# Kernel optimization log

Measured on AMD Instinct MI355X. Metric: run time of the kernel, lower is better.

The kernel has to match this reference:

```python
import jax, jax.numpy as jnp
import numpy as np

B, N, D, H, K = 8, 1024, 1024, 64, 20


def setup_inputs() -> dict:
    key = jax.random.key(0)
    ks = jax.random.split(key, 8)
    s = 0.05
    return {
        "f1": jax.random.normal(ks[0], (B, N, D), jnp.float32),
        "f2": jax.random.normal(ks[1], (B, N, D), jnp.float32),
        "W1a": jax.random.normal(ks[2], (D, H), jnp.float32) * s,
        "b1a": jnp.zeros((H,), jnp.float32),
        "W2a": jax.random.normal(ks[3], (H, H), jnp.float32) * s,
        "b2a": jnp.zeros((H,), jnp.float32),
        "W1b": jax.random.normal(ks[4], (H, H), jnp.float32) * s,
        "b1b": jnp.zeros((H,), jnp.float32),
        "W2b": jax.random.normal(ks[5], (H, H), jnp.float32) * s,
        "b2b": jnp.zeros((H,), jnp.float32),
        "k": K,
    }


def _knn_idx(f, k):
    # f: [N, D] -> indices [N, k] of k nearest neighbors (self excluded)
    sq = jnp.sum(f * f, axis=-1)                      # [N]
    d = sq[:, None] + sq[None, :] - 2.0 * (f @ f.T)   # [N, N] squared dists
    n = f.shape[0]
    d = d + jnp.eye(n, dtype=f.dtype) * jnp.float32(1e10)  # exclude self-loop
    _, idx = jax.lax.top_k(-d, k)                     # smallest distances
    return idx


def _gin_layer(x, idx, W1, b1, W2, b2):
    # GINConv with eps=0: MLP(x + sum_{j in N(i)} x_j)
    agg = jnp.sum(x[idx], axis=1)                     # [N, D] neighbor-sum
    h = x + agg
    h = jnp.maximum(h @ W1 + b1, 0.0) @ W2 + b2
    return h


def reference(f1, f2, W1a, b1a, W2a, b2a, W1b, b1b, W2b, b2b, k):
    def encode(f):
        idx = _knn_idx(f, k)
        h = _gin_layer(f, idx, W1a, b1a, W2a, b2a)
        h = _gin_layer(h, idx, W1b, b1b, W2b, b2b)
        return h

    def per_sample(a, b):
        z1 = encode(a)                                # [N, H]
        z2 = encode(b)                                # [N, H]
        sim = z1 @ z2.T                               # [N, N]
        return jax.nn.softmax(sim, axis=1)

    return jax.vmap(per_sample)(f1, f2)               # [B, N, N]
```

## Files before the change

### kernel.cpp

```cpp
#include <hip/hip_runtime.h>
#include <hip/hip_bf16.h>
#include <math.h>

#define BATCH 8
#define NPTS  1024
#define DIM   1024
#define HID   64
#define KNN   20
#define NMAT  16
#define KPACK 3072

typedef __attribute__((ext_vector_type(8))) short short8;
typedef __attribute__((ext_vector_type(4))) float floatx4;

__device__ __forceinline__ const float* mat_base(const float* f1, const float* f2, int m) {
    return (m < BATCH) ? (f1 + (size_t)m * NPTS * DIM)
                       : (f2 + (size_t)(m - BATCH) * NPTS * DIM);
}

__device__ __forceinline__ unsigned short f2bf_bits(float v) {
    __hip_bfloat16 h = __float2bfloat16(v);
    return *(unsigned short*)&h;
}
__device__ __forceinline__ float bfbits2f(unsigned short b) {
    union { unsigned u; float f; } c; c.u = ((unsigned)b) << 16; return c.f;
}

__global__ __launch_bounds__(256) void split_kernel(const float* __restrict__ f1,
                                                    const float* __restrict__ f2,
                                                    unsigned short* __restrict__ H,
                                                    float* __restrict__ sq) {
    int tid = threadIdx.x;
    int wave = tid >> 6, lane = tid & 63;
    int row = blockIdx.x * 4 + wave;
    int m = row >> 10, i = row & (NPTS - 1);
    const float* fr = mat_base(f1, f2, m) + (size_t)i * DIM;
    unsigned short* Hr = H + (size_t)row * KPACK;
    float s = 0.f;
    #pragma unroll
    for (int t = 0; t < 4; ++t) {
        int idx = t * 256 + lane * 4;
        float4 v = *(const float4*)&fr[idx];
        s += v.x * v.x + v.y * v.y + v.z * v.z + v.w * v.w;
        unsigned short h1[4], h2[4], h3[4];
        float vv[4] = {v.x, v.y, v.z, v.w};
        #pragma unroll
        for (int c = 0; c < 4; ++c) {
            unsigned short b1 = f2bf_bits(vv[c]);
            float r1 = vv[c] - bfbits2f(b1);
            unsigned short b2 = f2bf_bits(r1);
            float r2 = r1 - bfbits2f(b2);
            unsigned short b3 = f2bf_bits(r2);
            h1[c] = b1; h2[c] = b2; h3[c] = b3;
        }
        *(ushort4*)&Hr[idx]        = *(ushort4*)&h1[0];
        *(ushort4*)&Hr[1024 + idx] = *(ushort4*)&h2[0];
        *(ushort4*)&Hr[2048 + idx] = *(ushort4*)&h3[0];
    }
    #pragma unroll
    for (int o = 32; o > 0; o >>= 1) s += __shfl_down(s, o);
    if (lane == 0) sq[row] = s;
}

__global__ __launch_bounds__(256) void gram_mfma_kernel(const unsigned short* __restrict__ H,
                                                        const float* __restrict__ sq,
                                                        float* __restrict__ dist) {
    int bid = blockIdx.x;
    int xcd = bid & 7;
    int g = bid >> 3;
    int m = xcd + 8 * (g & 1);
    int t = g >> 1;
    int bi = 0;
    { int a = t; while (a >= 8 - bi) { a -= 8 - bi; ++bi; } t = a; }
    int bj = bi + t;
    int ti = bi << 7, tj = bj << 7;

    const unsigned short* Hm = H + (size_t)m * NPTS * KPACK;

    __shared__ __align__(16) unsigned short Asl[24 * 512];
    __shared__ __align__(16) unsigned short Bsl[24 * 512];

    int tid = threadIdx.x;
    int w = tid >> 6, lane = tid & 63;
    int wi = w >> 1, wj = w & 1;
    int r16 = lane & 15, kc = lane >> 4;

    floatx4 acc[4][4];
    #pragma unroll
    for (int a = 0; a < 4; ++a)
        #pragma unroll
        for (int b = 0; b < 4; ++b) acc[a][b] = (floatx4)0.f;

    for (int kk = 0; kk < 1024; kk += 32) {
        __syncthreads();
        #pragma unroll
        for (int c = 0; c < 6; ++c) {
            int ca = w * 6 + c;
            int seg = ca >> 3;
            int rb  = ca & 7;
            size_t koff = (size_t)(seg << 10) + kk + kc * 8;
            const unsigned short* ga = Hm + (size_t)(ti + rb * 16 + r16) * KPACK + koff;
            const unsigned short* gb = Hm + (size_t)(tj + rb * 16 + r16) * KPACK + koff;
            __builtin_amdgcn_global_load_lds(
                (const __attribute__((address_space(1))) void*)ga,
                (__attribute__((address_space(3))) void*)&Asl[ca * 512], 16, 0, 0);
            __builtin_amdgcn_global_load_lds(
                (const __attribute__((address_space(1))) void*)gb,
                (__attribute__((address_space(3))) void*)&Bsl[ca * 512], 16, 0, 0);
        }
        __syncthreads();
        short8 af[3][4];
        #pragma unroll
        for (int s = 0; s < 3; ++s)
            #pragma unroll
            for (int a = 0; a < 4; ++a)
                af[s][a] = *(const short8*)&Asl[(s * 8 + wi * 4 + a) * 512 + lane * 8];
        #pragma unroll
        for (int sb = 0; sb < 3; ++sb) {
            short8 bf[4];
            #pragma unroll
            for (int b = 0; b < 4; ++b)
                bf[b] = *(const short8*)&Bsl[(sb * 8 + wj * 4 + b) * 512 + lane * 8];
            #pragma unroll
            for (int sa = 0; sa < 3; ++sa) {
                if (sa + sb > 2) continue;
                #pragma unroll
                for (int a = 0; a < 4; ++a)
                    #pragma unroll
                    for (int b = 0; b < 4; ++b)
                        acc[a][b] = __builtin_amdgcn_mfma_f32_16x16x32_bf16(af[sa][a], bf[b], acc[a][b], 0, 0, 0);
            }
        }
    }

    const float* sqm = sq + m * NPTS;
    #pragma unroll
    for (int a = 0; a < 4; ++a) {
        int i0 = ti + wi * 64 + a * 16 + (lane >> 4) * 4;
        #pragma unroll
        for (int b = 0; b < 4; ++b) {
            int j = tj + wj * 64 + b * 16 + (lane & 15);
            float sqj = sqm[j];
            #pragma unroll
            for (int r = 0; r < 4; ++r) {
                int i = i0 + r;
                float v = sqm[i] + sqj - 2.f * acc[a][b][r];
                if (i == j) v += 1e10f;
                dist[((size_t)m * NPTS + i) * NPTS + j] = v;
                if (bi != bj) dist[((size_t)m * NPTS + j) * NPTS + i] = v;
            }
        }
    }
}

__global__ __launch_bounds__(256) void topk_kernel(const float* __restrict__ dist,
                                                   int* __restrict__ knn_idx) {
    int tid = threadIdx.x;
    int wave = tid >> 6, lane = tid & 63;
    int row = blockIdx.x * 4 + wave;
    const float* d = dist + (size_t)row * NPTS;
    float v[16];
    #pragma unroll
    for (int s = 0; s < 16; ++s) v[s] = d[s * 64 + lane];
    int myj = 0;
    for (int sel = 0; sel < KNN; ++sel) {
        float bv = v[0]; int bs = 0;
        #pragma unroll
        for (int s = 1; s < 16; ++s)
            if (v[s] < bv) { bv = v[s]; bs = s; }
        int bj = bs * 64 + lane;
        #pragma unroll
        for (int off = 1; off < 64; off <<= 1) {
            float ov = __shfl_xor(bv, off);
            int   oj = __shfl_xor(bj, off);
            if (ov < bv || (ov == bv && oj < bj)) { bv = ov; bj = oj; }
        }
        if ((bj & 63) == lane) v[bj >> 6] = 3e38f;
        if (lane == sel) myj = bj;
    }
    if (lane < KNN) knn_idx[(size_t)row * KNN + lane] = myj;
}

__global__ __launch_bounds__(256) void hsum_big_kernel(const float* __restrict__ f1,
                                                       const float* __restrict__ f2,
                                                       const int* __restrict__ knn_idx,
                                                       float* __restrict__ hsum) {
    int bid = blockIdx.x;
    int xcd = bid & 7;
    int g = bid >> 3;
    int m = xcd + 8 * (g >> 10);
    int i = g & 1023;
    int row = m * NPTS + i;
    const float* f = mat_base(f1, f2, m);
    __shared__ int nb[KNN];
    int tid = threadIdx.x;
    if (tid < KNN) nb[tid] = knn_idx[(size_t)row * KNN + tid];
    __syncthreads();
    int c = tid * 4;
    float4 acc = *(const float4*)&f[(size_t)i * DIM + c];
    #pragma unroll
    for (int t = 0; t < KNN; ++t) {
        float4 v = *(const float4*)&f[(size_t)nb[t] * DIM + c];
        acc.x += v.x; acc.y += v.y; acc.z += v.z; acc.w += v.w;
    }
    *(float4*)&hsum[(size_t)row * DIM + c] = acc;
}

__global__ __launch_bounds__(256) void hsum_small_kernel(const float* __restrict__ h,
                                                         const int* __restrict__ knn_idx,
                                                         float* __restrict__ outp) {
    int tid = threadIdx.x;
    int wave = tid >> 6, lane = tid & 63;
    int row = blockIdx.x * 4 + wave;
    int m = row >> 10;
    const int* nb = knn_idx + (size_t)row * KNN;
    const float* hm = h + (size_t)m * NPTS * HID;
    float acc = h[(size_t)row * HID + lane];
    #pragma unroll
    for (int t = 0; t < KNN; ++t)
        acc += hm[(size_t)nb[t] * HID + lane];
    outp[(size_t)row * HID + lane] = acc;
}

template <int DIN, bool RELU>
__global__ __launch_bounds__(256) void mlp_gemm_kernel(const float* __restrict__ A,
                                                       const float* __restrict__ W,
                                                       const float* __restrict__ bias,
                                                       float* __restrict__ C) {
    int row0 = blockIdx.x * 64;
    __shared__ float As[64][20];
    __shared__ float Ws[16][HID];
    int tid = threadIdx.x;
    int ty = tid >> 4, tx = tid & 15;
    float acc[4][4];
    #pragma unroll
    for (int i = 0; i < 4; ++i)
        #pragma unroll
        for (int j = 0; j < 4; ++j) acc[i][j] = 0.f;
    for (int kk = 0; kk < DIN; kk += 16) {
        {
            int r = tid >> 2, c = (tid & 3) * 4;
            *(float4*)&As[r][c] = *(const float4*)&A[(size_t)(row0 + r) * DIN + kk + c];
        }
        {
            int d = tid >> 4, hh = (tid & 15) * 4;
            *(float4*)&Ws[d][hh] = *(const float4*)&W[(size_t)(kk + d) * HID + hh];
        }
        __syncthreads();
        #pragma unroll
        for (int k = 0; k < 16; ++k) {
            float a[4];
            #pragma unroll
            for (int ii = 0; ii < 4; ++ii) a[ii] = As[ty * 4 + ii][k];
            float4 w = *(const float4*)&Ws[k][tx * 4];
            #pragma unroll
            for (int ii = 0; ii < 4; ++ii) {
                acc[ii][0] += a[ii] * w.x;
                acc[ii][1] += a[ii] * w.y;
                acc[ii][2] += a[ii] * w.z;
                acc[ii][3] += a[ii] * w.w;
            }
        }
        __syncthreads();
    }
    #pragma unroll
    for (int ii = 0; ii < 4; ++ii) {
        int r = row0 + ty * 4 + ii;
        float o[4];
        #pragma unroll
        for (int jj = 0; jj < 4; ++jj) {
            float v = acc[ii][jj] + bias[tx * 4 + jj];
            if (RELU) v = fmaxf(v, 0.f);
            o[jj] = v;
        }
        *(float4*)&C[(size_t)r * HID + tx * 4] = *(float4*)&o[0];
    }
}

__global__ __launch_bounds__(256) void sim_kernel(const float* __restrict__ z,
                                                  float* __restrict__ logits) {
    int bid = blockIdx.x;
    int b = bid >> 8;
    int tile = bid & 255;
    int ti = (tile >> 4) << 6;
    int tj = (tile & 15) << 6;
    const float* z1 = z + (size_t)b * NPTS * HID;
    const float* z2 = z + (size_t)(BATCH + b) * NPTS * HID;
    __shared__ float Z1[64][68];
    __shared__ float Z2[64][68];
    int tid = threadIdx.x;
    #pragma unroll
    for (int i = 0; i < 4; ++i) {
        int l = tid + i * 256;
        int r = l >> 4, c = (l & 15) * 4;
        *(float4*)&Z1[r][c] = *(const float4*)&z1[(size_t)(ti + r) * HID + c];
        *(float4*)&Z2[r][c] = *(const float4*)&z2[(size_t)(tj + r) * HID + c];
    }
    __syncthreads();
    int ty = tid >> 4, tx = tid & 15;
    float acc[4][4];
    #pragma unroll
    for (int i = 0; i < 4; ++i)
        #pragma unroll
        for (int j = 0; j < 4; ++j) acc[i][j] = 0.f;
    #pragma unroll
    for (int h = 0; h < HID; ++h) {
        float a[4], bb[4];
        #pragma unroll
        for (int ii = 0; ii < 4; ++ii) { a[ii] = Z1[ty * 4 + ii][h]; bb[ii] = Z2[tx * 4 + ii][h]; }
        #pragma unroll
        for (int ii = 0; ii < 4; ++ii)
            #pragma unroll
            for (int jj = 0; jj < 4; ++jj)
                acc[ii][jj] += a[ii] * bb[jj];
    }
    #pragma unroll
    for (int ii = 0; ii < 4; ++ii) {
        float* dst = logits + ((size_t)b * NPTS + ti + ty * 4 + ii) * NPTS + tj + tx * 4;
        *(float4*)&dst[0] = *(float4*)&acc[ii][0];
    }
}

__global__ __launch_bounds__(256) void softmax_kernel(const float* __restrict__ logits,
                                                      float* __restrict__ out) {
    int row = blockIdx.x;
    const float* L = logits + (size_t)row * NPTS;
    __shared__ float buf[NPTS];
    __shared__ float red[8];
    int tid = threadIdx.x;
    int wave = tid >> 6, lane = tid & 63;
    float mx = -3e38f;
    #pragma unroll
    for (int s = 0; s < 4; ++s) {
        float v = L[tid + s * 256];
        buf[tid + s * 256] = v;
        mx = fmaxf(mx, v);
    }
    #pragma unroll
    for (int off = 32; off > 0; off >>= 1) mx = fmaxf(mx, __shfl_down(mx, off));
    if (lane == 0) red[wave] = mx;
    __syncthreads();
    mx = fmaxf(fmaxf(red[0], red[1]), fmaxf(red[2], red[3]));
    float sum = 0.f;
    #pragma unroll
    for (int s = 0; s < 4; ++s) {
        float e = expf(buf[tid + s * 256] - mx);
        buf[tid + s * 256] = e;
        sum += e;
    }
    #pragma unroll
    for (int off = 32; off > 0; off >>= 1) sum += __shfl_down(sum, off);
    if (lane == 0) red[4 + wave] = sum;
    __syncthreads();
    float inv = 1.f / (red[4] + red[5] + red[6] + red[7]);
    #pragma unroll
    for (int s = 0; s < 4; ++s)
        out[(size_t)row * NPTS + tid + s * 256] = buf[tid + s * 256] * inv;
}

extern "C" void kernel_launch(void* const* d_in, const int* in_sizes, int n_in,
                              void* d_out, int out_size, void* d_ws, size_t ws_size,
                              hipStream_t stream) {
    const float* f1  = (const float*)d_in[0];
    const float* f2  = (const float*)d_in[1];
    const float* W1a = (const float*)d_in[2];
    const float* b1a = (const float*)d_in[3];
    const float* W2a = (const float*)d_in[4];
    const float* b2a = (const float*)d_in[5];
    const float* W1b = (const float*)d_in[6];
    const float* b1b = (const float*)d_in[7];
    const float* W2b = (const float*)d_in[8];
    const float* b2b = (const float*)d_in[9];
    float* out = (float*)d_out;

    char* ws = (char*)d_ws;
    unsigned short* H = (unsigned short*)ws;
    float* dist = (float*)(ws + (size_t)NMAT * NPTS * KPACK * sizeof(unsigned short));
    float* sq   = dist + (size_t)NMAT * NPTS * NPTS;
    int*   kidx = (int*)(sq + NMAT * NPTS);
    float* bufA = (float*)(kidx + NMAT * NPTS * KNN);
    float* bufB = bufA + (size_t)NMAT * NPTS * HID;

    split_kernel<<<NMAT * NPTS / 4, 256, 0, stream>>>(f1, f2, H, sq);
    gram_mfma_kernel<<<NMAT * 36, 256, 0, stream>>>(H, sq, dist);
    topk_kernel<<<NMAT * NPTS / 4, 256, 0, stream>>>(dist, kidx);
    hsum_big_kernel<<<NMAT * NPTS, 256, 0, stream>>>(f1, f2, kidx, dist);
    mlp_gemm_kernel<DIM, true><<<NMAT * NPTS / 64, 256, 0, stream>>>(dist, W1a, b1a, bufA);
    mlp_gemm_kernel<HID, false><<<NMAT * NPTS / 64, 256, 0, stream>>>(bufA, W2a, b2a, bufB);
    hsum_small_kernel<<<NMAT * NPTS / 4, 256, 0, stream>>>(bufB, kidx, bufA);
    mlp_gemm_kernel<HID, true><<<NMAT * NPTS / 64, 256, 0, stream>>>(bufA, W1b, b1b, bufB);
    mlp_gemm_kernel<HID, false><<<NMAT * NPTS / 64, 256, 0, stream>>>(bufB, W2b, b2b, bufA);
    sim_kernel<<<BATCH * 256, 256, 0, stream>>>(bufA, dist);
    softmax_kernel<<<BATCH * NPTS, 256, 0, stream>>>(dist, out);
}
```

Measured before the change: 587.0 us.

## Project features to hidden dim before neighbor aggregation and fuse GIN stages

Result: faster. 540.9 us (-7.9%).

```diff
diff --git a/kernel.cpp b/kernel.cpp
--- a/kernel.cpp
+++ b/kernel.cpp
@@ -181,53 +181,13 @@
     if (lane < KNN) knn_idx[(size_t)row * KNN + lane] = myj;
 }
 
-__global__ __launch_bounds__(256) void hsum_big_kernel(const float* __restrict__ f1,
-                                                       const float* __restrict__ f2,
-                                                       const int* __restrict__ knn_idx,
-                                                       float* __restrict__ hsum) {
-    int bid = blockIdx.x;
-    int xcd = bid & 7;
-    int g = bid >> 3;
-    int m = xcd + 8 * (g >> 10);
-    int i = g & 1023;
-    int row = m * NPTS + i;
-    const float* f = mat_base(f1, f2, m);
-    __shared__ int nb[KNN];
-    int tid = threadIdx.x;
-    if (tid < KNN) nb[tid] = knn_idx[(size_t)row * KNN + tid];
-    __syncthreads();
-    int c = tid * 4;
-    float4 acc = *(const float4*)&f[(size_t)i * DIM + c];
-    #pragma unroll
-    for (int t = 0; t < KNN; ++t) {
-        float4 v = *(const float4*)&f[(size_t)nb[t] * DIM + c];
-        acc.x += v.x; acc.y += v.y; acc.z += v.z; acc.w += v.w;
-    }
-    *(float4*)&hsum[(size_t)row * DIM + c] = acc;
-}
-
-__global__ __launch_bounds__(256) void hsum_small_kernel(const float* __restrict__ h,
-                                                         const int* __restrict__ knn_idx,
-                                                         float* __restrict__ outp) {
-    int tid = threadIdx.x;
-    int wave = tid >> 6, lane = tid & 63;
-    int row = blockIdx.x * 4 + wave;
-    int m = row >> 10;
-    const int* nb = knn_idx + (size_t)row * KNN;
-    const float* hm = h + (size_t)m * NPTS * HID;
-    float acc = h[(size_t)row * HID + lane];
-    #pragma unroll
-    for (int t = 0; t < KNN; ++t)
-        acc += hm[(size_t)nb[t] * HID + lane];
-    outp[(size_t)row * HID + lane] = acc;
-}
-
-template <int DIN, bool RELU>
-__global__ __launch_bounds__(256) void mlp_gemm_kernel(const float* __restrict__ A,
-                                                       const float* __restrict__ W,
-                                                       const float* __restrict__ bias,
-                                                       float* __restrict__ C) {
+__global__ __launch_bounds__(256) void ymlp_kernel(const float* __restrict__ f1,
+                                                   const float* __restrict__ f2,
+                                                   const float* __restrict__ W,
+                                                   float* __restrict__ y) {
     int row0 = blockIdx.x * 64;
+    int m = row0 >> 10;
+    const float* A = mat_base(f1, f2, m) + (size_t)(row0 & (NPTS - 1)) * DIM;
     __shared__ float As[64][20];
     __shared__ float Ws[16][HID];
     int tid = threadIdx.x;
@@ -237,10 +197,10 @@
     for (int i = 0; i < 4; ++i)
         #pragma unroll
         for (int j = 0; j < 4; ++j) acc[i][j] = 0.f;
-    for (int kk = 0; kk < DIN; kk += 16) {
+    for (int kk = 0; kk < DIM; kk += 16) {
         {
             int r = tid >> 2, c = (tid & 3) * 4;
-            *(float4*)&As[r][c] = *(const float4*)&A[(size_t)(row0 + r) * DIN + kk + c];
+            *(float4*)&As[r][c] = *(const float4*)&A[(size_t)r * DIM + kk + c];
         }
         {
             int d = tid >> 4, hh = (tid & 15) * 4;
@@ -264,16 +224,173 @@
         __syncthreads();
     }
     #pragma unroll
+    for (int ii = 0; ii < 4; ++ii)
+        *(float4*)&y[(size_t)(row0 + ty * 4 + ii) * HID + tx * 4] = *(float4*)&acc[ii][0];
+}
+
+__global__ __launch_bounds__(256) void t1h1_kernel(const float* __restrict__ y,
+                                                   const int* __restrict__ knn_idx,
+                                                   const float* __restrict__ W,
+                                                   const float* __restrict__ bias1,
+                                                   const float* __restrict__ bias2,
+                                                   float* __restrict__ h1) {
+    int row0 = blockIdx.x * 64;
+    int m = row0 >> 10;
+    __shared__ int nb[64 * KNN];
+    __shared__ float t1s[64][65];
+    __shared__ float Ws[64][HID];
+    __shared__ float b1s[HID], b2s[HID];
+    int tid = threadIdx.x;
+    for (int k = tid; k < 64 * KNN; k += 256) nb[k] = knn_idx[(size_t)row0 * KNN + k];
+    for (int k = tid; k < 64 * HID; k += 256) Ws[k >> 6][k & 63] = W[k];
+    if (tid < HID) { b1s[tid] = bias1[tid]; b2s[tid] = bias2[tid]; }
+    __syncthreads();
+    {
+        int r = tid >> 2, c0 = (tid & 3) * 16;
+        const float* yr = y + (size_t)(row0 + r) * HID + c0;
+        float4 a[4];
+        #pragma unroll
+        for (int q = 0; q < 4; ++q) a[q] = *(const float4*)&yr[q * 4];
+        const float* ym = y + (size_t)(m << 10) * HID;
+        #pragma unroll
+        for (int t = 0; t < KNN; ++t) {
+            const float* yn = ym + (size_t)nb[r * KNN + t] * HID + c0;
+            #pragma unroll
+            for (int q = 0; q < 4; ++q) {
+                float4 v = *(const float4*)&yn[q * 4];
+                a[q].x += v.x; a[q].y += v.y; a[q].z += v.z; a[q].w += v.w;
+            }
+        }
+        #pragma unroll
+        for (int q = 0; q < 4; ++q) {
+            int c = c0 + q * 4;
+            t1s[r][c + 0] = fmaxf(a[q].x + b1s[c + 0], 0.f);
+            t1s[r][c + 1] = fmaxf(a[q].y + b1s[c + 1], 0.f);
+            t1s[r][c + 2] = fmaxf(a[q].z + b1s[c + 2], 0.f);
+            t1s[r][c + 3] = fmaxf(a[q].w + b1s[c + 3], 0.f);
+        }
+    }
+    __syncthreads();
+    int ty = tid >> 4, tx = tid & 15;
+    float acc[4][4];
+    #pragma unroll
+    for (int i = 0; i < 4; ++i)
+        #pragma unroll
+        for (int j = 0; j < 4; ++j) acc[i][j] = 0.f;
+    #pragma unroll
+    for (int k = 0; k < HID; ++k) {
+        float a[4];
+        #pragma unroll
+        for (int ii = 0; ii < 4; ++ii) a[ii] = t1s[ty * 4 + ii][k];
+        float4 w = *(const float4*)&Ws[k][tx * 4];
+        #pragma unroll
+        for (int ii = 0; ii < 4; ++ii) {
+            acc[ii][0] += a[ii] * w.x;
+            acc[ii][1] += a[ii] * w.y;
+            acc[ii][2] += a[ii] * w.z;
+            acc[ii][3] += a[ii] * w.w;
+        }
+    }
+    #pragma unroll
     for (int ii = 0; ii < 4; ++ii) {
-        int r = row0 + ty * 4 + ii;
         float o[4];
         #pragma unroll
-        for (int jj = 0; jj < 4; ++jj) {
-            float v = acc[ii][jj] + bias[tx * 4 + jj];
-            if (RELU) v = fmaxf(v, 0.f);
-            o[jj] = v;
-        }
-        *(float4*)&C[(size_t)r * HID + tx * 4] = *(float4*)&o[0];
+        for (int jj = 0; jj < 4; ++jj) o[jj] = acc[ii][jj] + b2s[tx * 4 + jj];
+        *(float4*)&h1[(size_t)(row0 + ty * 4 + ii) * HID + tx * 4] = *(float4*)&o[0];
+    }
+}
+
+__global__ __launch_bounds__(256) void t2z_kernel(const float* __restrict__ h1,
+                                                  const int* __restrict__ knn_idx,
+                                                  const float* __restrict__ W1,
+                                                  const float* __restrict__ bias1,
+                                                  const float* __restrict__ W2,
+                                                  const float* __restrict__ bias2,
+                                                  float* __restrict__ z) {
+    int row0 = blockIdx.x * 64;
+    int m = row0 >> 10;
+    __shared__ int nb[64 * KNN];
+    __shared__ float hs[64][65];
+    __shared__ float t2s[64][65];
+    __shared__ float Ws[64][HID];
+    __shared__ float b1s[HID], b2s[HID];
+    int tid = threadIdx.x;
+    for (int k = tid; k < 64 * KNN; k += 256) nb[k] = knn_idx[(size_t)row0 * KNN + k];
+    for (int k = tid; k < 64 * HID; k += 256) Ws[k >> 6][k & 63] = W1[k];
+    if (tid < HID) { b1s[tid] = bias1[tid]; b2s[tid] = bias2[tid]; }
+    __syncthreads();
+    {
+        int r = tid >> 2, c0 = (tid & 3) * 16;
+        const float* hr = h1 + (size_t)(row0 + r) * HID + c0;
+        float4 a[4];
+        #pragma unroll
+        for (int q = 0; q < 4; ++q) a[q] = *(const float4*)&hr[q * 4];
+        const float* hm = h1 + (size_t)(m << 10) * HID;
+        #pragma unroll
+        for (int t = 0; t < KNN; ++t) {
+            const float* hn = hm + (size_t)nb[r * KNN + t] * HID + c0;
+            #pragma unroll
+            for (int q = 0; q < 4; ++q) {
+                float4 v = *(const float4*)&hn[q * 4];
+                a[q].x += v.x; a[q].y += v.y; a[q].z += v.z; a[q].w += v.w;
+            }
+        }
+        #pragma unroll
+        for (int q = 0; q < 4; ++q) *(float4*)&hs[r][c0 + q * 4] = a[q];
+    }
+    __syncthreads();
+    int ty = tid >> 4, tx = tid & 15;
+    float acc[4][4];
+    #pragma unroll
+    for (int i = 0; i < 4; ++i)
+        #pragma unroll
+        for (int j = 0; j < 4; ++j) acc[i][j] = 0.f;
+    #pragma unroll
+    for (int k = 0; k < HID; ++k) {
+        float a[4];
+        #pragma unroll
+        for (int ii = 0; ii < 4; ++ii) a[ii] = hs[ty * 4 + ii][k];
+        float4 w = *(const float4*)&Ws[k][tx * 4];
+        #pragma unroll
+        for (int ii = 0; ii < 4; ++ii) {
+            acc[ii][0] += a[ii] * w.x;
+            acc[ii][1] += a[ii] * w.y;
+            acc[ii][2] += a[ii] * w.z;
+            acc[ii][3] += a[ii] * w.w;
+        }
+    }
+    #pragma unroll
+    for (int ii = 0; ii < 4; ++ii)
+        #pragma unroll
+        for (int jj = 0; jj < 4; ++jj)
+            t2s[ty * 4 + ii][tx * 4 + jj] = fmaxf(acc[ii][jj] + b1s[tx * 4 + jj], 0.f);
+    __syncthreads();
+    for (int k = tid; k < 64 * HID; k += 256) Ws[k >> 6][k & 63] = W2[k];
+    __syncthreads();
+    #pragma unroll
+    for (int i = 0; i < 4; ++i)
+        #pragma unroll
+        for (int j = 0; j < 4; ++j) acc[i][j] = 0.f;
+    #pragma unroll
+    for (int k = 0; k < HID; ++k) {
+        float a[4];
+        #pragma unroll
+        for (int ii = 0; ii < 4; ++ii) a[ii] = t2s[ty * 4 + ii][k];
+        float4 w = *(const float4*)&Ws[k][tx * 4];
+        #pragma unroll
+        for (int ii = 0; ii < 4; ++ii) {
+            acc[ii][0] += a[ii] * w.x;
+            acc[ii][1] += a[ii] * w.y;
+            acc[ii][2] += a[ii] * w.z;
+            acc[ii][3] += a[ii] * w.w;
+        }
+    }
+    #pragma unroll
+    for (int ii = 0; ii < 4; ++ii) {
+        float o[4];
+        #pragma unroll
+        for (int jj = 0; jj < 4; ++jj) o[jj] = acc[ii][jj] + b2s[tx * 4 + jj];
+        *(float4*)&z[(size_t)(row0 + ty * 4 + ii) * HID + tx * 4] = *(float4*)&o[0];
     }
 }
 
@@ -378,18 +495,16 @@
     float* dist = (float*)(ws + (size_t)NMAT * NPTS * KPACK * sizeof(unsigned short));
     float* sq   = dist + (size_t)NMAT * NPTS * NPTS;
     int*   kidx = (int*)(sq + NMAT * NPTS);
-    float* bufA = (float*)(kidx + NMAT * NPTS * KNN);
-    float* bufB = bufA + (size_t)NMAT * NPTS * HID;
+    float* ybuf = (float*)(kidx + NMAT * NPTS * KNN);
+    float* h1b  = ybuf + (size_t)NMAT * NPTS * HID;
+    float* zb   = h1b + (size_t)NMAT * NPTS * HID;
 
     split_kernel<<<NMAT * NPTS / 4, 256, 0, stream>>>(f1, f2, H, sq);
     gram_mfma_kernel<<<NMAT * 36, 256, 0, stream>>>(H, sq, dist);
     topk_kernel<<<NMAT * NPTS / 4, 256, 0, stream>>>(dist, kidx);
-    hsum_big_kernel<<<NMAT * NPTS, 256, 0, stream>>>(f1, f2, kidx, dist);
-    mlp_gemm_kernel<DIM, true><<<NMAT * NPTS / 64, 256, 0, stream>>>(dist, W1a, b1a, bufA);
-    mlp_gemm_kernel<HID, false><<<NMAT * NPTS / 64, 256, 0, stream>>>(bufA, W2a, b2a, bufB);
-    hsum_small_kernel<<<NMAT * NPTS / 4, 256, 0, stream>>>(bufB, kidx, bufA);
-    mlp_gemm_kernel<HID, true><<<NMAT * NPTS / 64, 256, 0, stream>>>(bufA, W1b, b1b, bufB);
-    mlp_gemm_kernel<HID, false><<<NMAT * NPTS / 64, 256, 0, stream>>>(bufB, W2b, b2b, bufA);
-    sim_kernel<<<BATCH * 256, 256, 0, stream>>>(bufA, dist);
+    ymlp_kernel<<<NMAT * NPTS / 64, 256, 0, stream>>>(f1, f2, W1a, ybuf);
+    t1h1_kernel<<<NMAT * NPTS / 64, 256, 0, stream>>>(ybuf, kidx, W2a, b1a, b2a, h1b);
+    t2z_kernel<<<NMAT * NPTS / 64, 256, 0, stream>>>(h1b, kidx, W1b, b1b, W2b, b2b, zb);
+    sim_kernel<<<BATCH * 256, 256, 0, stream>>>(zb, dist);
     softmax_kernel<<<BATCH * NPTS, 256, 0, stream>>>(dist, out);
 }
```
